# Kernel tuning notes

Measured on AMD Instinct MI355X. Metric: run time of the kernel, lower is better.

Reference implementation:

```python
import jax, jax.numpy as jnp
import numpy as np

B, N, M, D, NHEAD, FF, C, K = 2, 16384, 2048, 256, 8, 512, 50, 3
HID = 128          # embed/pos hidden
HEAD_HID = 256     # seg head hidden
L = 4              # depth
EPS = 1e-5


def setup_inputs() -> dict:
    key = jax.random.key(0)
    ks = jax.random.split(key, 32)
    g = lambda i, shape: jax.random.normal(ks[i], shape, dtype=jnp.float32) * 0.02
    z = lambda shape: jnp.zeros(shape, jnp.float32)
    o = lambda shape: jnp.ones(shape, jnp.float32)
    return {
        "xyz": jax.random.normal(ks[0], (B, N, 3), dtype=jnp.float32),
        "embed_w1": g(1, (3, HID)), "embed_b1": z((HID,)),
        "embed_w2": g(2, (HID, D)), "embed_b2": z((D,)),
        "pos_w1": g(3, (3, HID)), "pos_b1": z((HID,)),
        "pos_w2": g(4, (HID, D)), "pos_b2": z((D,)),
        "Wq": g(5, (L, D, D)), "bq": z((L, D)),
        "Wk": g(6, (L, D, D)), "bk": z((L, D)),
        "Wv": g(7, (L, D, D)), "bv": z((L, D)),
        "Wo": g(8, (L, D, D)), "bo": z((L, D)),
        "ln1_s": o((L, D)), "ln1_b": z((L, D)),
        "W1": g(9, (L, D, FF)), "b1": z((L, FF)),
        "W2": g(10, (L, FF, D)), "b2": z((L, D)),
        "ln2_s": o((L, D)), "ln2_b": z((L, D)),
        "head_w1": g(11, (D, HEAD_HID)), "head_b1": z((HEAD_HID,)),
        "head_w2": g(12, (HEAD_HID, C)), "head_b2": z((C,)),
    }


def _ln(x, s, b):
    m = x.mean(-1, keepdims=True)
    v = ((x - m) ** 2).mean(-1, keepdims=True)
    return (x - m) / jnp.sqrt(v + EPS) * s + b


def reference(xyz, embed_w1, embed_b1, embed_w2, embed_b2,
              pos_w1, pos_b1, pos_w2, pos_b2,
              Wq, bq, Wk, bk, Wv, bv, Wo, bo, ln1_s, ln1_b,
              W1, b1, W2, b2, ln2_s, ln2_b,
              head_w1, head_b1, head_w2, head_b2):
    # deterministic token subsample (replaces randperm stub): strided pick of M points
    stride = N // M
    tok = xyz[:, ::stride, :][:, :M]                                  # [B,M,3]
    # per-point embed + learned positional encoding
    x = jax.nn.relu(tok @ embed_w1 + embed_b1) @ embed_w2 + embed_b2  # [B,M,D]
    x = x + jax.nn.relu(tok @ pos_w1 + pos_b1) @ pos_w2 + pos_b2
    dh = D // NHEAD
    scale = 1.0 / jnp.sqrt(jnp.float32(dh))

    def layer(x, p):
        wq, bq_, wk, bk_, wv, bv_, wo, bo_, l1s, l1b, w1, b1_, w2, b2_, l2s, l2b = p
        # pre-norm MHSA
        y = _ln(x, l1s, l1b)
        q = (y @ wq + bq_).reshape(B, M, NHEAD, dh)
        k = (y @ wk + bk_).reshape(B, M, NHEAD, dh)
        v = (y @ wv + bv_).reshape(B, M, NHEAD, dh)
        att = jax.nn.softmax(jnp.einsum('bqhd,bkhd->bhqk', q, k) * scale, axis=-1)
        o = jnp.einsum('bhqk,bkhd->bqhd', att, v).reshape(B, M, D)
        x = x + o @ wo + bo_
        # pre-norm FFN (gelu, exact erf as in torch)
        y = _ln(x, l2s, l2b)
        x = x + jax.nn.gelu(y @ w1 + b1_, approximate=False) @ w2 + b2_
        return x, None

    x, _ = jax.lax.scan(layer, x, (Wq, bq, Wk, bk, Wv, bv, Wo, bo,
                                   ln1_s, ln1_b, W1, b1, W2, b2, ln2_s, ln2_b))
    logits_tok = jax.nn.relu(x @ head_w1 + head_b1) @ head_w2 + head_b2  # [B,M,C]

    # kNN propagation N->M: dist^2 = |q|^2 + |k|^2 - 2 q.k, topk smallest
    q2 = (xyz ** 2).sum(-1)[..., None]            # [B,N,1]
    k2 = (tok ** 2).sum(-1)[:, None, :]           # [B,1,M]
    dist = q2 + k2 - 2.0 * jnp.einsum('bnd,bmd->bnm', xyz, tok)
    dist = jax.lax.stop_gradient(jnp.maximum(dist, 0.0))
    idx = jax.lax.top_k(-dist, K)[1]              # [B,N,K]
    logits_nk = logits_tok[jnp.arange(B)[:, None, None], idx]  # [B,N,K,C]
    return logits_nk.mean(axis=2)                 # [B,N,C]
```

## Files before the change

kernel.cpp:

```cpp
#include <hip/hip_runtime.h>
#include <hip/hip_bf16.h>
#include <math.h>

#define B_ 2
#define N_ 16384
#define M_ 2048
#define D_ 256
#define NHEAD_ 8
#define DH_ 32
#define FF_ 512
#define C_ 50
#define HID_ 128
#define HHID_ 256
#define L_ 4
#define EPS_ 1e-5f
#define TOK_ (B_*M_)
#define QSCALE_ 0.25507604155757994f

typedef short short8 __attribute__((ext_vector_type(8)));
typedef float f32x4 __attribute__((ext_vector_type(4)));

__device__ __forceinline__ short f2bf(float f) {
  union { float f; unsigned u; } c; c.f = f;
  unsigned u = c.u;
  unsigned r = (u + 0x7FFFu + ((u >> 16) & 1u)) >> 16;
  return (short)r;
}
__device__ __forceinline__ unsigned pack2bf(float a, float b) {
  return ((unsigned)(unsigned short)f2bf(a)) | (((unsigned)(unsigned short)f2bf(b)) << 16);
}
__device__ __forceinline__ float fast_exp2(float x) {
  float r;
  asm("v_exp_f32 %0, %1" : "=v"(r) : "v"(x));
  return r;
}
__device__ __forceinline__ unsigned cvt_pk_bf16(float lo, float hi) {
  unsigned r;
  asm("v_cvt_pk_bf16_f32 %0, %1, %2" : "=v"(r) : "v"(lo), "v"(hi));
  return r;
}

__global__ __launch_bounds__(128) void embed_kernel(
    const float* __restrict__ xyz,
    const float* __restrict__ ew1, const float* __restrict__ eb1,
    const float* __restrict__ ew2, const float* __restrict__ eb2,
    const float* __restrict__ pw1, const float* __restrict__ pb1,
    const float* __restrict__ pw2, const float* __restrict__ pb2,
    float* __restrict__ x) {
  int t = blockIdx.x;
  int b = t / M_, m = t % M_;
  const float* p = xyz + ((size_t)b * N_ + (size_t)m * 8) * 3;
  float t0 = p[0], t1 = p[1], t2 = p[2];
  __shared__ float he[HID_], hp[HID_];
  int j = threadIdx.x;
  {
    float a = fmaf(t0, ew1[j], fmaf(t1, ew1[HID_ + j], fmaf(t2, ew1[2 * HID_ + j], eb1[j])));
    he[j] = fmaxf(a, 0.f);
    float c = fmaf(t0, pw1[j], fmaf(t1, pw1[HID_ + j], fmaf(t2, pw1[2 * HID_ + j], pb1[j])));
    hp[j] = fmaxf(c, 0.f);
  }
  __syncthreads();
  for (int d = j; d < D_; d += HID_) {
    float acc = eb2[d] + pb2[d];
    for (int k = 0; k < HID_; ++k) {
      acc = fmaf(he[k], ew2[k * D_ + d], acc);
      acc = fmaf(hp[k], pw2[k * D_ + d], acc);
    }
    x[(size_t)t * D_ + d] = acc;
  }
}

__global__ __launch_bounds__(256) void ln_kernel(
    const float* __restrict__ x, const float* __restrict__ s,
    const float* __restrict__ bb, float* __restrict__ y) {
  int r = blockIdx.x * 4 + (threadIdx.x >> 6);
  int t = threadIdx.x & 63;
  const float4* xr = (const float4*)(x + (size_t)r * D_);
  float4 v = xr[t];
  float sum = v.x + v.y + v.z + v.w;
  #pragma unroll
  for (int o = 1; o < 64; o <<= 1) sum += __shfl_xor(sum, o, 64);
  float mean = sum * (1.f / D_);
  float dx = v.x - mean, dy = v.y - mean, dz = v.z - mean, dw = v.w - mean;
  float vs = dx * dx + dy * dy + dz * dz + dw * dw;
  #pragma unroll
  for (int o = 1; o < 64; o <<= 1) vs += __shfl_xor(vs, o, 64);
  float inv = 1.0f / sqrtf(vs * (1.f / D_) + EPS_);
  float4 sv = ((const float4*)s)[t];
  float4 bv = ((const float4*)bb)[t];
  float4 out;
  out.x = dx * inv * sv.x + bv.x;
  out.y = dy * inv * sv.y + bv.y;
  out.z = dz * inv * sv.z + bv.z;
  out.w = dw * inv * sv.w + bv.w;
  ((float4*)(y + (size_t)r * D_))[t] = out;
}

__global__ __launch_bounds__(256) void head2_kernel(
    const float* __restrict__ y, const float* __restrict__ w2,
    const float* __restrict__ b2, float* __restrict__ lt) {
  __shared__ float ys[4][HHID_];
  int w = threadIdx.x >> 6, l = threadIdx.x & 63;
  int t = blockIdx.x * 4 + w;
  float4 v = ((const float4*)(y + (size_t)t * HHID_))[l];
  *(float4*)&ys[w][l * 4] = v;
  int c = l < C_ ? l : 0;
  float a0 = 0.f, a1 = 0.f, a2 = 0.f, a3 = 0.f;
  #pragma unroll 4
  for (int k = 0; k < HHID_; k += 4) {
    a0 = fmaf(ys[w][k + 0], w2[(k + 0) * C_ + c], a0);
    a1 = fmaf(ys[w][k + 1], w2[(k + 1) * C_ + c], a1);
    a2 = fmaf(ys[w][k + 2], w2[(k + 2) * C_ + c], a2);
    a3 = fmaf(ys[w][k + 3], w2[(k + 3) * C_ + c], a3);
  }
  if (l < C_) lt[(size_t)t * C_ + l] = (a0 + a1) + (a2 + a3) + b2[l];
}

template <int ACT, int RES>
__device__ __forceinline__ void gemm_body(
    const float* __restrict__ A, const float* __restrict__ W,
    const float* __restrict__ bias, const float* __restrict__ R,
    float* __restrict__ Cc, short* __restrict__ out16, float oscale,
    int K, int Ncols, int m0, int n0) {
  __shared__ short As[32][40];
  __shared__ short Bs[64][40];
  int tid = threadIdx.x;
  int w = tid >> 6, l = tid & 63;
  int lq = l & 15, lg = l >> 4;
  int wr = (w & 1) * 16, wc = (w >> 1) * 32;
  int ar = tid >> 3, ak = (tid & 7) * 4;
  int wn = tid & 63, wk = (tid >> 6) * 8;
  f32x4 acc0 = {0.f, 0.f, 0.f, 0.f};
  f32x4 acc1 = {0.f, 0.f, 0.f, 0.f};
  for (int kk = 0; kk < K; kk += 32) {
    __syncthreads();
    {
      float4 a4 = *(const float4*)(A + (size_t)(m0 + ar) * K + kk + ak);
      uint2 au;
      au.x = pack2bf(a4.x, a4.y);
      au.y = pack2bf(a4.z, a4.w);
      *(uint2*)&As[ar][ak] = au;
      const float* wp = W + (size_t)(kk + wk) * Ncols + n0 + wn;
      float w0 = wp[0];
      float w1 = wp[(size_t)Ncols];
      float w2 = wp[2 * (size_t)Ncols];
      float w3 = wp[3 * (size_t)Ncols];
      float w4 = wp[4 * (size_t)Ncols];
      float w5 = wp[5 * (size_t)Ncols];
      float w6 = wp[6 * (size_t)Ncols];
      float w7 = wp[7 * (size_t)Ncols];
      uint4 wu;
      wu.x = pack2bf(w0, w1); wu.y = pack2bf(w2, w3);
      wu.z = pack2bf(w4, w5); wu.w = pack2bf(w6, w7);
      *(uint4*)&Bs[wn][wk] = wu;
    }
    __syncthreads();
    short8 af = *(short8*)&As[wr + lq][lg * 8];
    short8 b0 = *(short8*)&Bs[wc + lq][lg * 8];
    short8 b1 = *(short8*)&Bs[wc + 16 + lq][lg * 8];
    acc0 = __builtin_amdgcn_mfma_f32_16x16x32_bf16(af, b0, acc0, 0, 0, 0);
    acc1 = __builtin_amdgcn_mfma_f32_16x16x32_bf16(af, b1, acc1, 0, 0, 0);
  }
  int row = m0 + wr + lg * 4;
  #pragma unroll
  for (int r = 0; r < 4; ++r) {
    #pragma unroll
    for (int fj = 0; fj < 2; ++fj) {
      int col = n0 + wc + fj * 16 + lq;
      float v = (fj ? acc1[r] : acc0[r]) + bias[col];
      if (ACT == 1) v = fmaxf(v, 0.f);
      else if (ACT == 2) v = 0.5f * v * (1.f + erff(v * 0.70710678118654752f));
      if (RES) v += R[(size_t)(row + r) * Ncols + col];
      if (out16) out16[(size_t)(row + r) * Ncols + col] = f2bf(v * oscale);
      else Cc[(size_t)(row + r) * Ncols + col] = v;
    }
  }
}

template <int ACT, int RES>
__global__ __launch_bounds__(256) void gemm_mfma(
    const float* __restrict__ A, const float* __restrict__ W,
    const float* __restrict__ bias, const float* __restrict__ R,
    float* __restrict__ Cc, int K, int Ncols) {
  gemm_body<ACT, RES>(A, W, bias, R, Cc, nullptr, 1.f, K, Ncols, blockIdx.y * 32, blockIdx.x * 64);
}

__global__ __launch_bounds__(256) void qkv_mfma(
    const float* __restrict__ A,
    const float* __restrict__ Wq, const float* __restrict__ Wk, const float* __restrict__ Wv,
    const float* __restrict__ bq, const float* __restrict__ bk, const float* __restrict__ bv,
    short* __restrict__ q16, short* __restrict__ k16, float* __restrict__ vb) {
  int sel = blockIdx.x >> 2;
  int n0 = (blockIdx.x & 3) << 6;
  const float* W = sel == 0 ? Wq : (sel == 1 ? Wk : Wv);
  const float* bb = sel == 0 ? bq : (sel == 1 ? bk : bv);
  short* out16 = sel == 0 ? q16 : (sel == 1 ? k16 : nullptr);
  float oscale = sel == 0 ? QSCALE_ : 1.f;
  gemm_body<0, 0>(A, W, bb, nullptr, vb, out16, oscale, D_, D_, blockIdx.y * 32, n0);
}

__global__ __launch_bounds__(256) void vtrans_kernel(
    const float* __restrict__ vb, short* __restrict__ vt16) {
  int bid = blockIdx.x;
  int mt = bid & 31;
  int h = (bid >> 5) & 7;
  int b = bid >> 8;
  __shared__ short ts[64][34];
  int m0 = mt * 64;
  int tid = threadIdx.x;
  int mm = tid >> 2, dd = (tid & 3) * 8;
  const float* vp = vb + (size_t)(b * M_ + m0 + mm) * D_ + h * DH_ + dd;
  float4 a0 = ((const float4*)vp)[0];
  float4 a1 = ((const float4*)vp)[1];
  ts[mm][dd + 0] = f2bf(a0.x); ts[mm][dd + 1] = f2bf(a0.y);
  ts[mm][dd + 2] = f2bf(a0.z); ts[mm][dd + 3] = f2bf(a0.w);
  ts[mm][dd + 4] = f2bf(a1.x); ts[mm][dd + 5] = f2bf(a1.y);
  ts[mm][dd + 6] = f2bf(a1.z); ts[mm][dd + 7] = f2bf(a1.w);
  __syncthreads();
  int d = tid >> 3, mc = (tid & 7) * 8;
  short8 r;
  #pragma unroll
  for (int j = 0; j < 8; ++j) r[j] = ts[mc + j][d];
  *(short8*)&vt16[(size_t)((b * NHEAD_ + h) * DH_ + d) * M_ + m0 + mc] = r;
}

#define KSTR 40
#define VSTR 72
#define PSTR 72
__global__ __launch_bounds__(256) void attn_mfma_kernel(
    const short* __restrict__ q16, const short* __restrict__ k16,
    const short* __restrict__ vt16,
    float* __restrict__ po0, float* __restrict__ po1,
    float* __restrict__ po2, float* __restrict__ po3,
    float* __restrict__ pl) {
  __shared__ short Ks[64][KSTR];
  __shared__ short Vt[32][VSTR];
  __shared__ short Ps[4][16][PSTR];
  int bid = blockIdx.x;
  int quar = bid & 3;
  int qt = (bid >> 2) & 31;
  int h  = (bid >> 7) & 7;
  int b  = bid >> 10;
  int tid = threadIdx.x;
  int w  = tid >> 6;
  int l  = tid & 63;
  int lq = l & 15;
  int lg = l >> 4;

  short8 qf = *(const short8*)&q16[(size_t)(b * M_ + qt * 64 + w * 16 + lq) * D_ + h * DH_ + lg * 8];

  float l_i = 0.f;
  f32x4 o0 = {0.f, 0.f, 0.f, 0.f};
  f32x4 o1 = {0.f, 0.f, 0.f, 0.f};
  int srow = tid >> 2, scol = (tid & 3) * 8;
  int vd = tid >> 3, vm = (tid & 7) * 8;
  const short* kp = k16 + (size_t)(b * M_ + quar * 512 + srow) * D_ + h * DH_ + scol;
  const short* vp = vt16 + (size_t)((b * NHEAD_ + h) * DH_ + vd) * M_ + quar * 512 + vm;

  for (int kt = 0; kt < 8; ++kt) {
    __syncthreads();
    *(short8*)&Ks[srow][scol] = *(const short8*)(kp + (size_t)(kt * 64) * D_);
    *(short8*)&Vt[vd][vm]     = *(const short8*)(vp + kt * 64);
    __syncthreads();
    f32x4 st[4];
    #pragma unroll
    for (int t = 0; t < 4; ++t) {
      short8 kf = *(short8*)&Ks[t * 16 + lq][lg * 8];
      f32x4 z = {0.f, 0.f, 0.f, 0.f};
      st[t] = __builtin_amdgcn_mfma_f32_16x16x32_bf16(kf, qf, z, 0, 0, 0);
    }
    #pragma unroll
    for (int t = 0; t < 4; ++t)
      #pragma unroll
      for (int r2 = 0; r2 < 4; ++r2) {
        st[t][r2] = fast_exp2(st[t][r2]);
        l_i += st[t][r2];
      }
    {
      unsigned* pw = (unsigned*)&Ps[w][lq][0];
      #pragma unroll
      for (int t = 0; t < 4; ++t) {
        uint2 pk;
        pk.x = cvt_pk_bf16(st[t][0], st[t][1]);
        pk.y = cvt_pk_bf16(st[t][2], st[t][3]);
        *(uint2*)(pw + t * 8 + lg * 2) = pk;
      }
    }
    #pragma unroll
    for (int c = 0; c < 2; ++c) {
      short8 pf = *(short8*)&Ps[w][lq][c * 32 + lg * 8];
      short8 v0 = *(short8*)&Vt[lq][c * 32 + lg * 8];
      short8 v1 = *(short8*)&Vt[16 + lq][c * 32 + lg * 8];
      o0 = __builtin_amdgcn_mfma_f32_16x16x32_bf16(v0, pf, o0, 0, 0, 0);
      o1 = __builtin_amdgcn_mfma_f32_16x16x32_bf16(v1, pf, o1, 0, 0, 0);
    }
  }
  l_i += __shfl_xor(l_i, 16, 64);
  l_i += __shfl_xor(l_i, 32, 64);
  int f = (b * NHEAD_ + h) * M_ + qt * 64 + w * 16 + lq;
  float* pp = (quar == 0 ? po0 : quar == 1 ? po1 : quar == 2 ? po2 : po3) + (size_t)f * 32;
  #pragma unroll
  for (int r2 = 0; r2 < 4; ++r2) pp[lg * 4 + r2] = o0[r2];
  #pragma unroll
  for (int r2 = 0; r2 < 4; ++r2) pp[16 + lg * 4 + r2] = o1[r2];
  if (lg == 0) pl[quar * (16 * M_) + f] = l_i;
}

__global__ __launch_bounds__(256) void attn_combine(
    const float* __restrict__ po0, const float* __restrict__ po1,
    const float* __restrict__ po2, const float* __restrict__ po3,
    const float* __restrict__ pl, float* __restrict__ o) {
  int idx = blockIdx.x * 256 + threadIdx.x;
  int f = idx >> 3, dq = (idx & 7) * 4;
  float inv = 1.f / (pl[f] + pl[16 * M_ + f] + pl[32 * M_ + f] + pl[48 * M_ + f]);
  const float4 a = *(const float4*)&po0[(size_t)f * 32 + dq];
  const float4 c = *(const float4*)&po1[(size_t)f * 32 + dq];
  const float4 e = *(const float4*)&po2[(size_t)f * 32 + dq];
  const float4 g = *(const float4*)&po3[(size_t)f * 32 + dq];
  int b = f >> 14, h = (f >> 11) & 7, m = f & (M_ - 1);
  float4 r;
  r.x = (a.x + c.x + e.x + g.x) * inv;
  r.y = (a.y + c.y + e.y + g.y) * inv;
  r.z = (a.z + c.z + e.z + g.z) * inv;
  r.w = (a.w + c.w + e.w + g.w) * inv;
  *(float4*)&o[(size_t)(b * M_ + m) * D_ + h * DH_ + dq] = r;
}

__global__ __launch_bounds__(512) void knn_kernel(
    const float* __restrict__ xyz, const float* __restrict__ lt,
    float* __restrict__ out) {
  __shared__ float4 tok[2056];
  int b = blockIdx.x >> 8;
  int q0 = (blockIdx.x & 255) << 6;
  int tid = threadIdx.x;
  for (int i = tid; i < M_; i += 512) {
    const float* tp = xyz + ((size_t)b * N_ + (size_t)i * 8) * 3;
    float a = tp[0], bb = tp[1], cc = tp[2];
    tok[i + (i >> 8)] = make_float4(a, bb, cc, a * a + bb * bb + cc * cc);
  }
  __syncthreads();
  int qi = tid >> 3, sl = tid & 7;
  int n = q0 + qi;
  const float* qp = xyz + ((size_t)b * N_ + n) * 3;
  float qx = qp[0], qy = qp[1], qz = qp[2];
  float q2 = qx * qx + qy * qy + qz * qz;
  float dd0 = INFINITY, dd1 = INFINITY, dd2 = INFINITY;
  int ii0 = 0, ii1 = 0, ii2 = 0;
  const float4* cp = &tok[sl * 257];
  int mb = sl << 8;
  #pragma unroll 4
  for (int j = 0; j < 256; ++j) {
    float4 t = cp[j];
    float dot = fmaf(qx, t.x, fmaf(qy, t.y, qz * t.z));
    float d = fmaxf(q2 + t.w - 2.f * dot, 0.f);
    if (d < dd2) {
      int m = mb + j;
      if (d < dd1) {
        dd2 = dd1; ii2 = ii1;
        if (d < dd0) { dd1 = dd0; ii1 = ii0; dd0 = d; ii0 = m; }
        else         { dd1 = d;  ii1 = m; }
      } else         { dd2 = d;  ii2 = m; }
    }
  }
  auto insT = [&](float d, int i) {
    if (d < dd2 || (d == dd2 && i < ii2)) {
      if (d < dd1 || (d == dd1 && i < ii1)) {
        dd2 = dd1; ii2 = ii1;
        if (d < dd0 || (d == dd0 && i < ii0)) { dd1 = dd0; ii1 = ii0; dd0 = d; ii0 = i; }
        else { dd1 = d; ii1 = i; }
      } else { dd2 = d; ii2 = i; }
    }
  };
  #pragma unroll
  for (int off = 1; off < 8; off <<= 1) {
    float pd0 = __shfl_xor(dd0, off, 64); int pi0 = __shfl_xor(ii0, off, 64);
    float pd1 = __shfl_xor(dd1, off, 64); int pi1 = __shfl_xor(ii1, off, 64);
    float pd2 = __shfl_xor(dd2, off, 64); int pi2 = __shfl_xor(ii2, off, 64);
    insT(pd0, pi0); insT(pd1, pi1); insT(pd2, pi2);
  }
  const float* l0 = lt + ((size_t)b * M_ + ii0) * C_;
  const float* l1 = lt + ((size_t)b * M_ + ii1) * C_;
  const float* l2 = lt + ((size_t)b * M_ + ii2) * C_;
  float* op = out + ((size_t)b * N_ + n) * C_;
  for (int cc = sl; cc < C_; cc += 8)
    op[cc] = (l0[cc] + l1[cc] + l2[cc]) * (1.f / 3.f);
}

extern "C" void kernel_launch(void* const* d_in, const int* in_sizes, int n_in,
                              void* d_out, int out_size, void* d_ws, size_t ws_size,
                              hipStream_t stream) {
  const float* xyz  = (const float*)d_in[0];
  const float* ew1  = (const float*)d_in[1];
  const float* eb1  = (const float*)d_in[2];
  const float* ew2  = (const float*)d_in[3];
  const float* eb2  = (const float*)d_in[4];
  const float* pw1  = (const float*)d_in[5];
  const float* pb1  = (const float*)d_in[6];
  const float* pw2  = (const float*)d_in[7];
  const float* pb2  = (const float*)d_in[8];
  const float* Wq   = (const float*)d_in[9];
  const float* bq   = (const float*)d_in[10];
  const float* Wk   = (const float*)d_in[11];
  const float* bk   = (const float*)d_in[12];
  const float* Wv   = (const float*)d_in[13];
  const float* bv   = (const float*)d_in[14];
  const float* Wo   = (const float*)d_in[15];
  const float* bo   = (const float*)d_in[16];
  const float* ln1s = (const float*)d_in[17];
  const float* ln1b = (const float*)d_in[18];
  const float* W1   = (const float*)d_in[19];
  const float* b1   = (const float*)d_in[20];
  const float* W2   = (const float*)d_in[21];
  const float* b2   = (const float*)d_in[22];
  const float* ln2s = (const float*)d_in[23];
  const float* ln2b = (const float*)d_in[24];
  const float* hw1  = (const float*)d_in[25];
  const float* hb1  = (const float*)d_in[26];
  const float* hw2  = (const float*)d_in[27];
  const float* hb2  = (const float*)d_in[28];
  float* out = (float*)d_out;

  float* x  = (float*)d_ws;
  float* y  = x  + (size_t)TOK_ * D_;
  float* qb = y  + (size_t)TOK_ * D_;
  float* kb = qb + (size_t)TOK_ * D_;
  float* vb = kb + (size_t)TOK_ * D_;
  float* ob = vb + (size_t)TOK_ * D_;
  float* ff = ob + (size_t)TOK_ * D_;
  float* lt = ff + (size_t)TOK_ * FF_;

  short* qb16 = (short*)qb;
  short* kb16 = qb16 + (size_t)TOK_ * D_;
  short* vt16 = (short*)kb;
  float* po0 = y;
  float* po1 = vb;
  float* po2 = ff;
  float* po3 = ff + (size_t)TOK_ * D_;
  float* pl = lt;

  embed_kernel<<<TOK_, 128, 0, stream>>>(xyz, ew1, eb1, ew2, eb2, pw1, pb1, pw2, pb2, x);

  dim3 gQKV(12, TOK_ / 32);
  dim3 gD(D_ / 64, TOK_ / 32);
  dim3 gF(FF_ / 64, TOK_ / 32);
  for (int l = 0; l < L_; ++l) {
    const float* wq = Wq + (size_t)l * D_ * D_;
    const float* wk = Wk + (size_t)l * D_ * D_;
    const float* wv = Wv + (size_t)l * D_ * D_;
    const float* wo = Wo + (size_t)l * D_ * D_;
    ln_kernel<<<TOK_ / 4, 256, 0, stream>>>(x, ln1s + l * D_, ln1b + l * D_, y);
    qkv_mfma<<<gQKV, 256, 0, stream>>>(y, wq, wk, wv, bq + l * D_, bk + l * D_, bv + l * D_, qb16, kb16, vb);
    vtrans_kernel<<<512, 256, 0, stream>>>(vb, vt16);
    attn_mfma_kernel<<<2048, 256, 0, stream>>>(qb16, kb16, vt16, po0, po1, po2, po3, pl);
    attn_combine<<<1024, 256, 0, stream>>>(po0, po1, po2, po3, pl, ob);
    gemm_mfma<0, 1><<<gD, 256, 0, stream>>>(ob, wo, bo + l * D_, x, x, D_, D_);
    ln_kernel<<<TOK_ / 4, 256, 0, stream>>>(x, ln2s + l * D_, ln2b + l * D_, y);
    gemm_mfma<2, 0><<<gF, 256, 0, stream>>>(y, W1 + (size_t)l * D_ * FF_, b1 + l * FF_, nullptr, ff, D_, FF_);
    gemm_mfma<0, 1><<<gD, 256, 0, stream>>>(ff, W2 + (size_t)l * FF_ * D_, b2 + l * D_, x, x, FF_, D_);
  }
  gemm_mfma<1, 0><<<dim3(HHID_ / 64, TOK_ / 32), 256, 0, stream>>>(x, hw1, hb1, nullptr, y, D_, HHID_);
  head2_kernel<<<TOK_ / 4, 256, 0, stream>>>(y, hw2, hb2, lt);
  knn_kernel<<<512, 512, 0, stream>>>(xyz, lt, out);
}
```

Measured before the change: 415.7 us.

## Store activations and pre-transposed weights in bf16; rework kNN to two queries per thread

```diff
diff --git a/kernel.cpp b/kernel.cpp
--- a/kernel.cpp
+++ b/kernel.cpp
@@ -18,6 +18,7 @@
 #define QSCALE_ 0.25507604155757994f
 
 typedef short short8 __attribute__((ext_vector_type(8)));
+typedef short short4_t __attribute__((ext_vector_type(4)));
 typedef float f32x4 __attribute__((ext_vector_type(4)));
 
 __device__ __forceinline__ short f2bf(float f) {
@@ -26,9 +27,6 @@
   unsigned r = (u + 0x7FFFu + ((u >> 16) & 1u)) >> 16;
   return (short)r;
 }
-__device__ __forceinline__ unsigned pack2bf(float a, float b) {
-  return ((unsigned)(unsigned short)f2bf(a)) | (((unsigned)(unsigned short)f2bf(b)) << 16);
-}
 __device__ __forceinline__ float fast_exp2(float x) {
   float r;
   asm("v_exp_f32 %0, %1" : "=v"(r) : "v"(x));
@@ -38,6 +36,55 @@
   unsigned r;
   asm("v_cvt_pk_bf16_f32 %0, %1, %2" : "=v"(r) : "v"(lo), "v"(hi));
   return r;
+}
+
+__global__ __launch_bounds__(256) void wconv_all(
+    const float* __restrict__ Wq, const float* __restrict__ Wk,
+    const float* __restrict__ Wv, const float* __restrict__ Wo,
+    const float* __restrict__ W1, const float* __restrict__ W2,
+    const float* __restrict__ h1,
+    short* __restrict__ WqT, short* __restrict__ WkT,
+    short* __restrict__ WvT, short* __restrict__ WoT,
+    short* __restrict__ W1T, short* __restrict__ W2T, short* __restrict__ h1T) {
+  int bid = blockIdx.x;
+  const float* W; short* WT; int Kd, Nd, tn, tk;
+  if (bid < 256) {
+    int mat = bid >> 6, rem = bid & 63, l = rem >> 4, t = rem & 15;
+    W  = (mat == 0 ? Wq : mat == 1 ? Wk : mat == 2 ? Wv : Wo) + l * 65536;
+    WT = (mat == 0 ? WqT : mat == 1 ? WkT : mat == 2 ? WvT : WoT) + l * 65536;
+    Kd = 256; Nd = 256; tn = t & 3; tk = t >> 2;
+  } else if (bid < 384) {
+    int rem = bid - 256, l = rem >> 5, t = rem & 31;
+    W = W1 + l * 131072; WT = W1T + l * 131072;
+    Kd = 256; Nd = 512; tn = t & 7; tk = t >> 3;
+  } else if (bid < 512) {
+    int rem = bid - 384, l = rem >> 5, t = rem & 31;
+    W = W2 + l * 131072; WT = W2T + l * 131072;
+    Kd = 512; Nd = 256; tn = t & 3; tk = t >> 2;
+  } else {
+    int t = bid - 512;
+    W = h1; WT = h1T; Kd = 256; Nd = 256; tn = t & 3; tk = t >> 2;
+  }
+  int n0 = tn * 64, k0 = tk * 64;
+  __shared__ short ts[64][72];
+  int tid = threadIdx.x;
+  #pragma unroll
+  for (int i = 0; i < 4; ++i) {
+    int r = i * 16 + (tid >> 4);
+    int c4 = (tid & 15) * 4;
+    float4 v = *(const float4*)&W[(size_t)(k0 + r) * Nd + n0 + c4];
+    ts[c4 + 0][r] = f2bf(v.x);
+    ts[c4 + 1][r] = f2bf(v.y);
+    ts[c4 + 2][r] = f2bf(v.z);
+    ts[c4 + 3][r] = f2bf(v.w);
+  }
+  __syncthreads();
+  #pragma unroll
+  for (int i = 0; i < 2; ++i) {
+    int n = i * 32 + (tid >> 3);
+    int kc = (tid & 7) * 8;
+    *(short8*)&WT[(size_t)(n0 + n) * Kd + k0 + kc] = *(short8*)&ts[n][kc];
+  }
 }
 
 __global__ __launch_bounds__(128) void embed_kernel(
@@ -72,7 +119,7 @@
 
 __global__ __launch_bounds__(256) void ln_kernel(
     const float* __restrict__ x, const float* __restrict__ s,
-    const float* __restrict__ bb, float* __restrict__ y) {
+    const float* __restrict__ bb, short* __restrict__ y16) {
   int r = blockIdx.x * 4 + (threadIdx.x >> 6);
   int t = threadIdx.x & 63;
   const float4* xr = (const float4*)(x + (size_t)r * D_);
@@ -88,12 +135,12 @@
   float inv = 1.0f / sqrtf(vs * (1.f / D_) + EPS_);
   float4 sv = ((const float4*)s)[t];
   float4 bv = ((const float4*)bb)[t];
-  float4 out;
-  out.x = dx * inv * sv.x + bv.x;
-  out.y = dy * inv * sv.y + bv.y;
-  out.z = dz * inv * sv.z + bv.z;
-  out.w = dw * inv * sv.w + bv.w;
-  ((float4*)(y + (size_t)r * D_))[t] = out;
+  short4_t ov;
+  ov[0] = f2bf(dx * inv * sv.x + bv.x);
+  ov[1] = f2bf(dy * inv * sv.y + bv.y);
+  ov[2] = f2bf(dz * inv * sv.z + bv.z);
+  ov[3] = f2bf(dw * inv * sv.w + bv.w);
+  *(short4_t*)(y16 + (size_t)r * D_ + t * 4) = ov;
 }
 
 __global__ __launch_bounds__(256) void head2_kernel(
@@ -117,10 +164,10 @@
 }
 
 template <int ACT, int RES>
-__device__ __forceinline__ void gemm_body(
-    const float* __restrict__ A, const float* __restrict__ W,
+__device__ __forceinline__ void gemm16_body(
+    const short* __restrict__ A16, const short* __restrict__ WT,
     const float* __restrict__ bias, const float* __restrict__ R,
-    float* __restrict__ Cc, short* __restrict__ out16, float oscale,
+    float* __restrict__ C, short* __restrict__ C16, float oscale,
     int K, int Ncols, int m0, int n0) {
   __shared__ short As[32][40];
   __shared__ short Bs[64][40];
@@ -134,26 +181,8 @@
   f32x4 acc1 = {0.f, 0.f, 0.f, 0.f};
   for (int kk = 0; kk < K; kk += 32) {
     __syncthreads();
-    {
-      float4 a4 = *(const float4*)(A + (size_t)(m0 + ar) * K + kk + ak);
-      uint2 au;
-      au.x = pack2bf(a4.x, a4.y);
-      au.y = pack2bf(a4.z, a4.w);
-      *(uint2*)&As[ar][ak] = au;
-      const float* wp = W + (size_t)(kk + wk) * Ncols + n0 + wn;
-      float w0 = wp[0];
-      float w1 = wp[(size_t)Ncols];
-      float w2 = wp[2 * (size_t)Ncols];
-      float w3 = wp[3 * (size_t)Ncols];
-      float w4 = wp[4 * (size_t)Ncols];
-      float w5 = wp[5 * (size_t)Ncols];
-      float w6 = wp[6 * (size_t)Ncols];
-      float w7 = wp[7 * (size_t)Ncols];
-      uint4 wu;
-      wu.x = pack2bf(w0, w1); wu.y = pack2bf(w2, w3);
-      wu.z = pack2bf(w4, w5); wu.w = pack2bf(w6, w7);
-      *(uint4*)&Bs[wn][wk] = wu;
-    }
+    *(short4_t*)&As[ar][ak] = *(const short4_t*)&A16[(size_t)(m0 + ar) * K + kk + ak];
+    *(short8*)&Bs[wn][wk]   = *(const short8*)&WT[(size_t)(n0 + wn) * K + kk + wk];
     __syncthreads();
     short8 af = *(short8*)&As[wr + lq][lg * 8];
     short8 b0 = *(short8*)&Bs[wc + lq][lg * 8];
@@ -171,51 +200,49 @@
       if (ACT == 1) v = fmaxf(v, 0.f);
       else if (ACT == 2) v = 0.5f * v * (1.f + erff(v * 0.70710678118654752f));
       if (RES) v += R[(size_t)(row + r) * Ncols + col];
-      if (out16) out16[(size_t)(row + r) * Ncols + col] = f2bf(v * oscale);
-      else Cc[(size_t)(row + r) * Ncols + col] = v;
+      if (C)   C[(size_t)(row + r) * Ncols + col] = v;
+      if (C16) C16[(size_t)(row + r) * Ncols + col] = f2bf(v * oscale);
     }
   }
 }
 
 template <int ACT, int RES>
-__global__ __launch_bounds__(256) void gemm_mfma(
-    const float* __restrict__ A, const float* __restrict__ W,
+__global__ __launch_bounds__(256) void gemm16(
+    const short* __restrict__ A16, const short* __restrict__ WT,
     const float* __restrict__ bias, const float* __restrict__ R,
-    float* __restrict__ Cc, int K, int Ncols) {
-  gemm_body<ACT, RES>(A, W, bias, R, Cc, nullptr, 1.f, K, Ncols, blockIdx.y * 32, blockIdx.x * 64);
-}
-
-__global__ __launch_bounds__(256) void qkv_mfma(
-    const float* __restrict__ A,
-    const float* __restrict__ Wq, const float* __restrict__ Wk, const float* __restrict__ Wv,
+    float* __restrict__ C, short* __restrict__ C16,
+    int K, int Ncols) {
+  gemm16_body<ACT, RES>(A16, WT, bias, R, C, C16, 1.f, K, Ncols,
+                        blockIdx.y * 32, blockIdx.x * 64);
+}
+
+__global__ __launch_bounds__(256) void qkv16(
+    const short* __restrict__ A16,
+    const short* __restrict__ WqT, const short* __restrict__ WkT, const short* __restrict__ WvT,
     const float* __restrict__ bq, const float* __restrict__ bk, const float* __restrict__ bv,
-    short* __restrict__ q16, short* __restrict__ k16, float* __restrict__ vb) {
+    short* __restrict__ q16, short* __restrict__ k16, short* __restrict__ v16) {
   int sel = blockIdx.x >> 2;
   int n0 = (blockIdx.x & 3) << 6;
-  const float* W = sel == 0 ? Wq : (sel == 1 ? Wk : Wv);
+  const short* WT = sel == 0 ? WqT : (sel == 1 ? WkT : WvT);
   const float* bb = sel == 0 ? bq : (sel == 1 ? bk : bv);
-  short* out16 = sel == 0 ? q16 : (sel == 1 ? k16 : nullptr);
+  short* out16 = sel == 0 ? q16 : (sel == 1 ? k16 : v16);
   float oscale = sel == 0 ? QSCALE_ : 1.f;
-  gemm_body<0, 0>(A, W, bb, nullptr, vb, out16, oscale, D_, D_, blockIdx.y * 32, n0);
+  gemm16_body<0, 0>(A16, WT, bb, nullptr, nullptr, out16, oscale, D_, D_,
+                    blockIdx.y * 32, n0);
 }
 
 __global__ __launch_bounds__(256) void vtrans_kernel(
-    const float* __restrict__ vb, short* __restrict__ vt16) {
+    const short* __restrict__ v16, short* __restrict__ vt16) {
   int bid = blockIdx.x;
   int mt = bid & 31;
   int h = (bid >> 5) & 7;
   int b = bid >> 8;
-  __shared__ short ts[64][34];
+  __shared__ short ts[64][40];
   int m0 = mt * 64;
   int tid = threadIdx.x;
   int mm = tid >> 2, dd = (tid & 3) * 8;
-  const float* vp = vb + (size_t)(b * M_ + m0 + mm) * D_ + h * DH_ + dd;
-  float4 a0 = ((const float4*)vp)[0];
-  float4 a1 = ((const float4*)vp)[1];
-  ts[mm][dd + 0] = f2bf(a0.x); ts[mm][dd + 1] = f2bf(a0.y);
-  ts[mm][dd + 2] = f2bf(a0.z); ts[mm][dd + 3] = f2bf(a0.w);
-  ts[mm][dd + 4] = f2bf(a1.x); ts[mm][dd + 5] = f2bf(a1.y);
-  ts[mm][dd + 6] = f2bf(a1.z); ts[mm][dd + 7] = f2bf(a1.w);
+  *(short8*)&ts[mm][dd] =
+      *(const short8*)&v16[(size_t)(b * M_ + m0 + mm) * D_ + h * DH_ + dd];
   __syncthreads();
   int d = tid >> 3, mc = (tid & 7) * 8;
   short8 r;
@@ -309,7 +336,7 @@
 __global__ __launch_bounds__(256) void attn_combine(
     const float* __restrict__ po0, const float* __restrict__ po1,
     const float* __restrict__ po2, const float* __restrict__ po3,
-    const float* __restrict__ pl, float* __restrict__ o) {
+    const float* __restrict__ pl, short* __restrict__ ob16) {
   int idx = blockIdx.x * 256 + threadIdx.x;
   int f = idx >> 3, dq = (idx & 7) * 4;
   float inv = 1.f / (pl[f] + pl[16 * M_ + f] + pl[32 * M_ + f] + pl[48 * M_ + f]);
@@ -318,72 +345,110 @@
   const float4 e = *(const float4*)&po2[(size_t)f * 32 + dq];
   const float4 g = *(const float4*)&po3[(size_t)f * 32 + dq];
   int b = f >> 14, h = (f >> 11) & 7, m = f & (M_ - 1);
-  float4 r;
-  r.x = (a.x + c.x + e.x + g.x) * inv;
-  r.y = (a.y + c.y + e.y + g.y) * inv;
-  r.z = (a.z + c.z + e.z + g.z) * inv;
-  r.w = (a.w + c.w + e.w + g.w) * inv;
-  *(float4*)&o[(size_t)(b * M_ + m) * D_ + h * DH_ + dq] = r;
+  short4_t r;
+  r[0] = f2bf((a.x + c.x + e.x + g.x) * inv);
+  r[1] = f2bf((a.y + c.y + e.y + g.y) * inv);
+  r[2] = f2bf((a.z + c.z + e.z + g.z) * inv);
+  r[3] = f2bf((a.w + c.w + e.w + g.w) * inv);
+  *(short4_t*)&ob16[(size_t)(b * M_ + m) * D_ + h * DH_ + dq] = r;
 }
 
 __global__ __launch_bounds__(512) void knn_kernel(
     const float* __restrict__ xyz, const float* __restrict__ lt,
     float* __restrict__ out) {
-  __shared__ float4 tok[2056];
+  __shared__ float4 tok[2064];
   int b = blockIdx.x >> 8;
   int q0 = (blockIdx.x & 255) << 6;
   int tid = threadIdx.x;
   for (int i = tid; i < M_; i += 512) {
     const float* tp = xyz + ((size_t)b * N_ + (size_t)i * 8) * 3;
     float a = tp[0], bb = tp[1], cc = tp[2];
-    tok[i + (i >> 8)] = make_float4(a, bb, cc, a * a + bb * bb + cc * cc);
+    tok[i + (i >> 7)] = make_float4(a, bb, cc, a * a + bb * bb + cc * cc);
   }
   __syncthreads();
-  int qi = tid >> 3, sl = tid & 7;
-  int n = q0 + qi;
-  const float* qp = xyz + ((size_t)b * N_ + n) * 3;
-  float qx = qp[0], qy = qp[1], qz = qp[2];
-  float q2 = qx * qx + qy * qy + qz * qz;
-  float dd0 = INFINITY, dd1 = INFINITY, dd2 = INFINITY;
-  int ii0 = 0, ii1 = 0, ii2 = 0;
-  const float4* cp = &tok[sl * 257];
-  int mb = sl << 8;
-  #pragma unroll 4
-  for (int j = 0; j < 256; ++j) {
+  int g = tid >> 4, sl = tid & 15;
+  int na = q0 + g, nb = q0 + 32 + g;
+  const float* qpa = xyz + ((size_t)b * N_ + na) * 3;
+  const float* qpb = xyz + ((size_t)b * N_ + nb) * 3;
+  float qxa = qpa[0], qya = qpa[1], qza = qpa[2];
+  float qxb = qpb[0], qyb = qpb[1], qzb = qpb[2];
+  float q2a = qxa * qxa + qya * qya + qza * qza;
+  float q2b = qxb * qxb + qyb * qyb + qzb * qzb;
+  float a0 = INFINITY, a1 = INFINITY, a2 = INFINITY;
+  int ia0 = 0, ia1 = 0, ia2 = 0;
+  float e0 = INFINITY, e1 = INFINITY, e2 = INFINITY;
+  int ie0 = 0, ie1 = 0, ie2 = 0;
+  const float4* cp = &tok[sl * 129];
+  int mb0 = sl << 7;
+  #pragma unroll 2
+  for (int j = 0; j < 128; ++j) {
     float4 t = cp[j];
-    float dot = fmaf(qx, t.x, fmaf(qy, t.y, qz * t.z));
-    float d = fmaxf(q2 + t.w - 2.f * dot, 0.f);
-    if (d < dd2) {
-      int m = mb + j;
-      if (d < dd1) {
-        dd2 = dd1; ii2 = ii1;
-        if (d < dd0) { dd1 = dd0; ii1 = ii0; dd0 = d; ii0 = m; }
-        else         { dd1 = d;  ii1 = m; }
-      } else         { dd2 = d;  ii2 = m; }
-    }
-  }
-  auto insT = [&](float d, int i) {
-    if (d < dd2 || (d == dd2 && i < ii2)) {
-      if (d < dd1 || (d == dd1 && i < ii1)) {
-        dd2 = dd1; ii2 = ii1;
-        if (d < dd0 || (d == dd0 && i < ii0)) { dd1 = dd0; ii1 = ii0; dd0 = d; ii0 = i; }
-        else { dd1 = d; ii1 = i; }
-      } else { dd2 = d; ii2 = i; }
+    float dota = fmaf(qxa, t.x, fmaf(qya, t.y, qza * t.z));
+    float da = fmaxf(q2a + t.w - 2.f * dota, 0.f);
+    float dotb = fmaf(qxb, t.x, fmaf(qyb, t.y, qzb * t.z));
+    float db = fmaxf(q2b + t.w - 2.f * dotb, 0.f);
+    if (da < a2) {
+      bool c0 = da < a0, c1 = da < a1;
+      int m = mb0 + j;
+      a2 = c1 ? a1 : da;  ia2 = c1 ? ia1 : m;
+      float n1 = c1 ? da : a1; int nj1 = c1 ? m : ia1;
+      a1 = c0 ? a0 : n1;  ia1 = c0 ? ia0 : nj1;
+      a0 = c0 ? da : a0;  ia0 = c0 ? m : ia0;
+    }
+    if (db < e2) {
+      bool c0 = db < e0, c1 = db < e1;
+      int m = mb0 + j;
+      e2 = c1 ? e1 : db;  ie2 = c1 ? ie1 : m;
+      float n1 = c1 ? db : e1; int nj1 = c1 ? m : ie1;
+      e1 = c0 ? e0 : n1;  ie1 = c0 ? ie0 : nj1;
+      e0 = c0 ? db : e0;  ie0 = c0 ? m : ie0;
+    }
+  }
+  auto insA = [&](float d, int i) {
+    if (d < a2 || (d == a2 && i < ia2)) {
+      if (d < a1 || (d == a1 && i < ia1)) {
+        a2 = a1; ia2 = ia1;
+        if (d < a0 || (d == a0 && i < ia0)) { a1 = a0; ia1 = ia0; a0 = d; ia0 = i; }
+        else { a1 = d; ia1 = i; }
+      } else { a2 = d; ia2 = i; }
     }
   };
-  #pragma unroll
-  for (int off = 1; off < 8; off <<= 1) {
-    float pd0 = __shfl_xor(dd0, off, 64); int pi0 = __shfl_xor(ii0, off, 64);
-    float pd1 = __shfl_xor(dd1, off, 64); int pi1 = __shfl_xor(ii1, off, 64);
-    float pd2 = __shfl_xor(dd2, off, 64); int pi2 = __shfl_xor(ii2, off, 64);
-    insT(pd0, pi0); insT(pd1, pi1); insT(pd2, pi2);
-  }
-  const float* l0 = lt + ((size_t)b * M_ + ii0) * C_;
-  const float* l1 = lt + ((size_t)b * M_ + ii1) * C_;
-  const float* l2 = lt + ((size_t)b * M_ + ii2) * C_;
-  float* op = out + ((size_t)b * N_ + n) * C_;
-  for (int cc = sl; cc < C_; cc += 8)
-    op[cc] = (l0[cc] + l1[cc] + l2[cc]) * (1.f / 3.f);
+  auto insB = [&](float d, int i) {
+    if (d < e2 || (d == e2 && i < ie2)) {
+      if (d < e1 || (d == e1 && i < ie1)) {
+        e2 = e1; ie2 = ie1;
+        if (d < e0 || (d == e0 && i < ie0)) { e1 = e0; ie1 = ie0; e0 = d; ie0 = i; }
+        else { e1 = d; ie1 = i; }
+      } else { e2 = d; ie2 = i; }
+    }
+  };
+  #pragma unroll
+  for (int off = 1; off < 16; off <<= 1) {
+    float p0 = __shfl_xor(a0, off, 64); int pi0 = __shfl_xor(ia0, off, 64);
+    float p1 = __shfl_xor(a1, off, 64); int pi1 = __shfl_xor(ia1, off, 64);
+    float p2 = __shfl_xor(a2, off, 64); int pi2 = __shfl_xor(ia2, off, 64);
+    insA(p0, pi0); insA(p1, pi1); insA(p2, pi2);
+    float r0 = __shfl_xor(e0, off, 64); int ri0 = __shfl_xor(ie0, off, 64);
+    float r1 = __shfl_xor(e1, off, 64); int ri1 = __shfl_xor(ie1, off, 64);
+    float r2 = __shfl_xor(e2, off, 64); int ri2 = __shfl_xor(ie2, off, 64);
+    insB(r0, ri0); insB(r1, ri1); insB(r2, ri2);
+  }
+  {
+    const float* l0 = lt + ((size_t)b * M_ + ia0) * C_;
+    const float* l1 = lt + ((size_t)b * M_ + ia1) * C_;
+    const float* l2 = lt + ((size_t)b * M_ + ia2) * C_;
+    float* op = out + ((size_t)b * N_ + na) * C_;
+    for (int cc = sl; cc < C_; cc += 16)
+      op[cc] = (l0[cc] + l1[cc] + l2[cc]) * (1.f / 3.f);
+  }
+  {
+    const float* l0 = lt + ((size_t)b * M_ + ie0) * C_;
+    const float* l1 = lt + ((size_t)b * M_ + ie1) * C_;
+    const float* l2 = lt + ((size_t)b * M_ + ie2) * C_;
+    float* op = out + ((size_t)b * N_ + nb) * C_;
+    for (int cc = sl; cc < C_; cc += 16)
+      op[cc] = (l0[cc] + l1[cc] + l2[cc]) * (1.f / 3.f);
+  }
 }
 
 extern "C" void kernel_launch(void* const* d_in, const int* in_sizes, int n_in,
@@ -420,45 +485,50 @@
   const float* hb2  = (const float*)d_in[28];
   float* out = (float*)d_out;
 
-  float* x  = (float*)d_ws;
-  float* y  = x  + (size_t)TOK_ * D_;
-  float* qb = y  + (size_t)TOK_ * D_;
-  float* kb = qb + (size_t)TOK_ * D_;
-  float* vb = kb + (size_t)TOK_ * D_;
-  float* ob = vb + (size_t)TOK_ * D_;
-  float* ff = ob + (size_t)TOK_ * D_;
-  float* lt = ff + (size_t)TOK_ * FF_;
-
-  short* qb16 = (short*)qb;
-  short* kb16 = qb16 + (size_t)TOK_ * D_;
-  short* vt16 = (short*)kb;
+  float* x   = (float*)d_ws;
+  float* y   = x + 1048576;
+  float* po2 = y + 1048576;
+  float* po3 = po2 + 1048576;
+  float* lt  = po3 + 1048576;
+  short* y16 = (short*)(lt + 204800);
+  short* q16 = y16 + 1048576;
+  short* k16 = q16 + 1048576;
+  short* v16 = k16 + 1048576;
+  short* vt16 = v16 + 1048576;
+  short* ob16 = vt16 + 1048576;
+  short* x16  = ob16 + 1048576;
+  short* ff16 = x16 + 1048576;
+  short* WqT = ff16 + 2097152;
+  short* WkT = WqT + 262144;
+  short* WvT = WkT + 262144;
+  short* WoT = WvT + 262144;
+  short* W1T = WoT + 262144;
+  short* W2T = W1T + 524288;
+  short* h1T = W2T + 524288;
   float* po0 = y;
-  float* po1 = vb;
-  float* po2 = ff;
-  float* po3 = ff + (size_t)TOK_ * D_;
-  float* pl = lt;
-
+  float* po1 = (float*)ff16;
+  float* pl  = lt;
+
+  wconv_all<<<528, 256, 0, stream>>>(Wq, Wk, Wv, Wo, W1, W2, hw1,
+                                     WqT, WkT, WvT, WoT, W1T, W2T, h1T);
   embed_kernel<<<TOK_, 128, 0, stream>>>(xyz, ew1, eb1, ew2, eb2, pw1, pb1, pw2, pb2, x);
 
   dim3 gQKV(12, TOK_ / 32);
   dim3 gD(D_ / 64, TOK_ / 32);
   dim3 gF(FF_ / 64, TOK_ / 32);
   for (int l = 0; l < L_; ++l) {
-    const float* wq = Wq + (size_t)l * D_ * D_;
-    const float* wk = Wk + (size_t)l * D_ * D_;
-    const float* wv = Wv + (size_t)l * D_ * D_;
-    const float* wo = Wo + (size_t)l * D_ * D_;
-    ln_kernel<<<TOK_ / 4, 256, 0, stream>>>(x, ln1s + l * D_, ln1b + l * D_, y);
-    qkv_mfma<<<gQKV, 256, 0, stream>>>(y, wq, wk, wv, bq + l * D_, bk + l * D_, bv + l * D_, qb16, kb16, vb);
-    vtrans_kernel<<<512, 256, 0, stream>>>(vb, vt16);
-    attn_mfma_kernel<<<2048, 256, 0, stream>>>(qb16, kb16, vt16, po0, po1, po2, po3, pl);
-    attn_combine<<<1024, 256, 0, stream>>>(po0, po1, po2, po3, pl, ob);
-    gemm_mfma<0, 1><<<gD, 256, 0, stream>>>(ob, wo, bo + l * D_, x, x, D_, D_);
-    ln_kernel<<<TOK_ / 4, 256, 0, stream>>>(x, ln2s + l * D_, ln2b + l * D_, y);
-    gemm_mfma<2, 0><<<gF, 256, 0, stream>>>(y, W1 + (size_t)l * D_ * FF_, b1 + l * FF_, nullptr, ff, D_, FF_);
-    gemm_mfma<0, 1><<<gD, 256, 0, stream>>>(ff, W2 + (size_t)l * FF_ * D_, b2 + l * D_, x, x, FF_, D_);
-  }
-  gemm_mfma<1, 0><<<dim3(HHID_ / 64, TOK_ / 32), 256, 0, stream>>>(x, hw1, hb1, nullptr, y, D_, HHID_);
+    ln_kernel<<<TOK_ / 4, 256, 0, stream>>>(x, ln1s + l * D_, ln1b + l * D_, y16);
+    qkv16<<<gQKV, 256, 0, stream>>>(y16, WqT + l * 65536, WkT + l * 65536, WvT + l * 65536,
+                                    bq + l * D_, bk + l * D_, bv + l * D_, q16, k16, v16);
+    vtrans_kernel<<<512, 256, 0, stream>>>(v16, vt16);
+    attn_mfma_kernel<<<2048, 256, 0, stream>>>(q16, k16, vt16, po0, po1, po2, po3, pl);
+    attn_combine<<<1024, 256, 0, stream>>>(po0, po1, po2, po3, pl, ob16);
+    gemm16<0, 1><<<gD, 256, 0, stream>>>(ob16, WoT + l * 65536, bo + l * D_, x, x, nullptr, D_, D_);
+    ln_kernel<<<TOK_ / 4, 256, 0, stream>>>(x, ln2s + l * D_, ln2b + l * D_, y16);
+    gemm16<2, 0><<<gF, 256, 0, stream>>>(y16, W1T + l * 131072, b1 + l * FF_, nullptr, nullptr, ff16, D_, FF_);
+    gemm16<0, 1><<<gD, 256, 0, stream>>>(ff16, W2T + l * 131072, b2 + l * D_, x, x, x16, FF_, D_);
+  }
+  gemm16<1, 0><<<gD, 256, 0, stream>>>(x16, h1T, hb1, nullptr, y, nullptr, D_, HHID_);
   head2_kernel<<<TOK_ / 4, 256, 0, stream>>>(y, hw2, hb2, lt);
   knn_kernel<<<512, 512, 0, stream>>>(xyz, lt, out);
 }
```

New measurement: 411.1 us. About the same (-1.1%).
